# Performance work log

Measured on AMD Instinct MI355X. Metric: run time of the kernel, lower is better.

Reference implementation:

```python
import jax, jax.numpy as jnp
import numpy as np

B, P, M, N, H, K, EH = 16, 50, 512, 1024, 64, 20, 200


def setup_inputs() -> dict:
    key = jax.random.key(0)
    ks = jax.random.split(key, 16)
    b = jax.random.normal(ks[0], (B, P, M, 1), jnp.float32)
    A = jax.random.normal(ks[1], (1, P, M, N), jnp.float32) / np.float32(np.sqrt(M))
    # random undirected multigraph on P nodes, stored with both directions
    s = jax.random.randint(ks[2], (B, EH), 0, P)
    off = jax.random.randint(ks[3], (B, EH), 1, P)
    d = (s + off) % P
    edge_index = jnp.stack([jnp.concatenate([s, d], 1), jnp.concatenate([d, s], 1)], 1).astype(jnp.int32)  # [B,2,2*EH]

    def lin(k, fi, fo, scale=None):
        scale = np.float32(1.0 / np.sqrt(fi)) if scale is None else np.float32(scale)
        return jax.random.normal(k, (fi, fo), jnp.float32) * scale, jnp.zeros((fo,), jnp.float32)

    W_e1, b_e1 = lin(ks[4], P * M, P * H)
    W_e2, b_e2 = lin(ks[5], P * H, 2 * P * H)
    W_e3, b_e3 = lin(ks[6], 2 * P * H, 4 * P * H)
    W_c1, b_c1 = lin(ks[7], 4 * H, 2 * H)
    W_c2, b_c2 = lin(ks[8], 2 * H, 2 * H)
    W_f1, b_f1 = lin(ks[9], 2 * H, H)
    W_f2, _ = lin(ks[10], H, K * 4, scale=1e-3)
    b_f2 = jnp.full((K * 4,), -2.0, jnp.float32)  # mimics fc2 init (tiny weights, negative bias)
    max_param = jnp.array([0.01, 0.1, 0.1, 0.1], jnp.float32).reshape(1, 1, 1, 4)  # [alpha,tau,rho,eta]_max
    y0 = jax.random.normal(ks[11], (B, P, N, 1), jnp.float32) * 0.01
    u0 = jax.random.normal(ks[12], (B, P, N, 1), jnp.float32) * 0.01
    d0 = jax.random.normal(ks[13], (B, P, N, 1), jnp.float32) * 0.01
    return dict(b=b, A=A, edge_index=edge_index, max_param=max_param,
                W_e1=W_e1, b_e1=b_e1, W_e2=W_e2, b_e2=b_e2, W_e3=W_e3, b_e3=b_e3,
                W_c1=W_c1, b_c1=b_c1, W_c2=W_c2, b_c2=b_c2,
                W_f1=W_f1, b_f1=b_f1, W_f2=W_f2, b_f2=b_f2,
                y0=y0, u0=u0, d0=d0)


def _lrelu(x):
    return jax.nn.leaky_relu(x, 0.01)


def _gcn(x, s, d, W, bias):
    # GCNConv: sym-normalized propagation with self loops. x: [P,F]
    h = x @ W
    deg = jnp.zeros((x.shape[0],), x.dtype).at[d].add(1.0) + 1.0  # +1 self loop
    dinv = jax.lax.rsqrt(deg)
    agg = jnp.zeros_like(h).at[d].add(h[s] * (dinv[s] * dinv[d])[:, None])
    agg = agg + h * (dinv * dinv)[:, None]  # self-loop term
    return agg + bias


def _delta(y, s, d):
    # nested neighbor loop: for each directed edge (s,d): delta[s]+=y[s]-y[d]; delta[d]-=same
    diff = y[s] - y[d]  # [E,N,1]
    return jnp.zeros_like(y).at[s].add(diff).at[d].add(-diff)


def reference(b, A, edge_index, max_param,
              W_e1, b_e1, W_e2, b_e2, W_e3, b_e3,
              W_c1, b_c1, W_c2, b_c2, W_f1, b_f1, W_f2, b_f2,
              y0, u0, d0):
    Bb = b.shape[0]
    n = A.shape[3]
    k_steps = W_f2.shape[1] // 4
    src, dst = edge_index[:, 0], edge_index[:, 1]

    # ---- GNN hypernetwork ----
    x = b.reshape(Bb, -1)
    x = _lrelu(x @ W_e1 + b_e1)
    x = _lrelu(x @ W_e2 + b_e2)
    x = (x @ W_e3 + b_e3).reshape(Bb, P, -1)  # [B,P,4H]
    x = _lrelu(jax.vmap(lambda xf, s, d: _gcn(xf, s, d, W_c1, b_c1))(x, src, dst))
    x = _lrelu(jax.vmap(lambda xf, s, d: _gcn(xf, s, d, W_c2, b_c2))(x, src, dst))
    x = x.mean(axis=1)  # global_mean_pool over nodes
    x = _lrelu(x @ W_f1 + b_f1)
    hyp = (x @ W_f2 + b_f2).reshape(Bb, k_steps, 1, 4)
    hyp = jax.nn.sigmoid(jnp.cumsum(hyp, axis=1)) * max_param  # [B,K,1,4]
    hyp_scan = jnp.transpose(hyp, (1, 3, 0, 2))[..., None, None]  # [K,4,B,1,1,1]

    # ---- precompute ----
    A0 = A[0]  # [P,M,N]
    AtA = jnp.einsum('pmn,pmk->pnk', A0, A0)  # [P,N,N]
    Atb = jnp.einsum('pmn,bpmo->bpno', A0, b)  # [B,P,N,1]
    sum_nb = jax.vmap(lambda s: jnp.zeros((P,), b.dtype).at[s].add(1.0))(src)[:, :, None, None]  # [B,P,1,1]

    # ---- unrolled D-ADMM / DLASSO ----
    def step(carry, hk):
        y_k, U_k, dlt = carry
        alpha, tau, rho, eta = hk[0], hk[1], hk[2], hk[3]
        AtAy = jnp.einsum('pnk,bpko->bpno', AtA, y_k)
        g = AtAy - Atb + jnp.sign(y_k) * tau + U_k * sum_nb + dlt * rho
        y_n = y_k - alpha * g
        dlt_n = jax.vmap(_delta)(y_n, src, dst)
        U_n = U_k + dlt_n * eta
        return (y_n, U_n, dlt_n), y_n

    _, Y = jax.lax.scan(step, (y0, u0, d0), hyp_scan)
    return Y  # [K,B,P,N,1]
```

## Files before the change

### kernel.cpp

```cpp
#include <hip/hip_runtime.h>

namespace {
constexpr int NB = 16;
constexpr int NP = 50;
constexpr int NM = 512;
constexpr int NN = 1024;
constexpr int NK = 20;
constexpr long ASZ = (long)NP * NM * NN;
constexpr long YSZ = (long)NB * NP * NN;
}

typedef __attribute__((ext_vector_type(8))) short bf16x8;
typedef __attribute__((ext_vector_type(4))) float f32x4;

__device__ __forceinline__ float lrelu(float x){ return x > 0.f ? x : 0.01f*x; }
__device__ __forceinline__ float bfu(unsigned short x){
  unsigned v = ((unsigned)x) << 16;
  return __builtin_bit_cast(float, v);
}
__device__ __forceinline__ unsigned short f2bf(float f){
  unsigned u = __builtin_bit_cast(unsigned, f);
  u += 0x7fffu + ((u >> 16) & 1u);
  return (unsigned short)(u >> 16);
}
__device__ __forceinline__ long toff(int n, int kk){
  return (long)(n>>4)*16384 + (long)(kk>>5)*512 + (long)((n&15)*32 + ((kk>>3)&3)*8 + (kk&7));
}

__global__ __launch_bounds__(256) void k_prep(const float* __restrict__ A,
                      unsigned short* __restrict__ abfT){
  const int p = blockIdx.x, mt = blockIdx.y, nt = blockIdx.z;
  const int tid = threadIdx.x;
  __shared__ unsigned short tile[64][72];
  const int m0 = mt*64, n0 = nt*64;
  {
    int r = tid>>2, cs = (tid&3)*16;
    const float* src = A + ((long)p*NM + m0 + r)*NN + n0 + cs;
    unsigned short tmp[16];
    #pragma unroll
    for (int q=0;q<16;q+=4){
      float4 v = *(const float4*)(src+q);
      tmp[q+0]=f2bf(v.x); tmp[q+1]=f2bf(v.y); tmp[q+2]=f2bf(v.z); tmp[q+3]=f2bf(v.w);
    }
    #pragma unroll
    for (int q=0;q<16;q++) tile[r][cs+q] = tmp[q];
  }
  __syncthreads();
  {
    int r = tid>>2, cs = (tid&3)*16;
    unsigned short* dst = abfT + ((long)p*NN + n0 + r)*NM + m0 + cs;
    unsigned short tmp[16];
    #pragma unroll
    for (int q=0;q<16;q++) tmp[q] = tile[cs+q][r];
    #pragma unroll
    for (int q=0;q<16;q+=8) *(uint4*)(dst+q) = *(const uint4*)&tmp[q];
  }
}

__global__ void k_init(const float* __restrict__ y0, float* __restrict__ y,
                       unsigned short* __restrict__ ybf, int n){
  int e = (blockIdx.x*blockDim.x + threadIdx.x)*4;
  if (e >= n) return;
  float4 a = *(const float4*)(y0+e);
  *(float4*)(y+e) = a;
  ushort4 o; o.x=f2bf(a.x); o.y=f2bf(a.y); o.z=f2bf(a.z); o.w=f2bf(a.w);
  *(ushort4*)(ybf+e) = o;
}

__global__ __launch_bounds__(256) void k_e0(const float* __restrict__ u0,
      const float* __restrict__ d0, const float* __restrict__ atb,
      const float* __restrict__ snbg, const float* __restrict__ hypg,
      float* __restrict__ w, float* __restrict__ e){
  long i = ((long)blockIdx.x*256 + threadIdx.x)*4;
  if (i >= YSZ) return;
  long bp = i >> 10;
  int b = (int)(bp/NP), p = (int)(bp%NP);
  float sp = snbg[b*NP+p], rho = hypg[b*80 + 2];
  float4 uv = *(const float4*)(u0+i);
  float4 dv = *(const float4*)(d0+i);
  float4 av = *(const float4*)(atb+i);
  float4 wv, ev;
  wv.x = uv.x*sp - av.x; wv.y = uv.y*sp - av.y;
  wv.z = uv.z*sp - av.z; wv.w = uv.w*sp - av.w;
  ev.x = wv.x + dv.x*rho; ev.y = wv.y + dv.y*rho;
  ev.z = wv.z + dv.z*rho; ev.w = wv.w + dv.w*rho;
  *(float4*)(w+i) = wv;
  *(float4*)(e+i) = ev;
}

__global__ __launch_bounds__(256) void k_atb(const unsigned short* __restrict__ abfT,
                      const float* __restrict__ src, float* __restrict__ z){
  const int p = blockIdx.x;
  const int tid = threadIdx.x, wave = tid>>6, lane = tid&63;
  __shared__ unsigned short tlds[16][520];
  {
    int b = tid>>4, c0 = (tid&15)*8;
    const float* tr = src + ((long)b*NP + p)*NM;
    #pragma unroll
    for (int it=0; it<4; it++){
      float4 lo = *(const float4*)(tr + it*128 + c0);
      float4 hi = *(const float4*)(tr + it*128 + c0 + 4);
      unsigned short w[8];
      w[0]=f2bf(lo.x); w[1]=f2bf(lo.y); w[2]=f2bf(lo.z); w[3]=f2bf(lo.w);
      w[4]=f2bf(hi.x); w[5]=f2bf(hi.y); w[6]=f2bf(hi.z); w[7]=f2bf(hi.w);
      *(uint4*)&tlds[b][it*128 + c0] = *(const uint4*)w;
    }
  }
  __syncthreads();
  const int lr = lane&15, kg = lane>>4;
  const int nt0 = blockIdx.y*4 + wave;
  const int n0 = nt0*16, n1 = (nt0+32)*16;
  const unsigned short* b0 = abfT + ((long)p*NN + n0 + lr)*NM + kg*8;
  const unsigned short* b1 = abfT + ((long)p*NN + n1 + lr)*NM + kg*8;
  const unsigned short* tp = &tlds[lr][kg*8];
  f32x4 acc0a={0.f,0.f,0.f,0.f}, acc0b={0.f,0.f,0.f,0.f};
  f32x4 acc1a={0.f,0.f,0.f,0.f}, acc1b={0.f,0.f,0.f,0.f};
  #pragma unroll 4
  for (int ks=0; ks<16; ks+=2){
    bf16x8 t0 = *(const bf16x8*)(tp + ks*32);
    bf16x8 t1 = *(const bf16x8*)(tp + ks*32 + 32);
    bf16x8 b00 = *(const bf16x8*)(b0 + (long)ks*32);
    bf16x8 b01 = *(const bf16x8*)(b0 + (long)ks*32 + 32);
    bf16x8 b10 = *(const bf16x8*)(b1 + (long)ks*32);
    bf16x8 b11 = *(const bf16x8*)(b1 + (long)ks*32 + 32);
    acc0a = __builtin_amdgcn_mfma_f32_16x16x32_bf16(t0, b00, acc0a, 0, 0, 0);
    acc1a = __builtin_amdgcn_mfma_f32_16x16x32_bf16(t0, b10, acc1a, 0, 0, 0);
    acc0b = __builtin_amdgcn_mfma_f32_16x16x32_bf16(t1, b01, acc0b, 0, 0, 0);
    acc1b = __builtin_amdgcn_mfma_f32_16x16x32_bf16(t1, b11, acc1b, 0, 0, 0);
  }
  f32x4 acc0 = acc0a + acc0b;
  f32x4 acc1 = acc1a + acc1b;
  #pragma unroll
  for (int r=0;r<4;r++){
    int bb = kg*4 + r;
    z[((long)bb*NP + p)*NN + n0 + lr] = acc0[r];
    z[((long)bb*NP + p)*NN + n1 + lr] = acc1[r];
  }
}

__global__ __launch_bounds__(256) void k_ata(const unsigned short* __restrict__ abfT,
                      unsigned short* __restrict__ ata){
  const int p = blockIdx.y;
  int yy = blockIdx.x, bi = 0;
  while (yy >= 8 - bi){ yy -= 8 - bi; bi++; }
  const int bj = bi + yy;
  const int i0 = bi*128, j0 = bj*128;
  const int tid = threadIdx.x, wave = tid>>6, lane = tid&63;
  const int lr = lane&15, kg = lane>>4;
  __shared__ unsigned short pa[128][72];
  __shared__ unsigned short pb[128][72];
  f32x4 acc[2][8];
  #pragma unroll
  for (int ti=0;ti<2;ti++)
    #pragma unroll
    for (int tj=0;tj<8;tj++) acc[ti][tj] = (f32x4){0.f,0.f,0.f,0.f};
  const unsigned short* Abase = abfT + (long)p*NN*NM;
  for (int mc=0; mc<NM; mc+=64){
    __syncthreads();
    {
      int r = tid>>1, c0 = (tid&1)*32;
      const unsigned short* sa = Abase + (long)(i0 + r)*NM + mc + c0;
      const unsigned short* sb = Abase + (long)(j0 + r)*NM + mc + c0;
      #pragma unroll
      for (int q=0;q<32;q+=8){
        *(uint4*)&pa[r][c0+q] = *(const uint4*)(sa+q);
        *(uint4*)&pb[r][c0+q] = *(const uint4*)(sb+q);
      }
    }
    __syncthreads();
    #pragma unroll
    for (int ks=0; ks<2; ks++){
      bf16x8 av0 = *(const bf16x8*)&pa[wave*32      + lr][ks*32 + kg*8];
      bf16x8 av1 = *(const bf16x8*)&pa[wave*32 + 16 + lr][ks*32 + kg*8];
      #pragma unroll
      for (int tj=0;tj<8;tj++){
        bf16x8 bv = *(const bf16x8*)&pb[tj*16 + lr][ks*32 + kg*8];
        acc[0][tj] = __builtin_amdgcn_mfma_f32_16x16x32_bf16(av0, bv, acc[0][tj], 0,0,0);
        acc[1][tj] = __builtin_amdgcn_mfma_f32_16x16x32_bf16(av1, bv, acc[1][tj], 0,0,0);
      }
    }
  }
  const long pbase = (long)p << 20;
  #pragma unroll
  for (int ti=0; ti<2; ti++){
    const int ib = i0 + wave*32 + ti*16;
    #pragma unroll
    for (int tj=0; tj<8; tj++){
      const int jb = j0 + tj*16;
      unsigned short w[4];
      #pragma unroll
      for (int r=0;r<4;r++) w[r] = f2bf(acc[ti][tj][r]);
      #pragma unroll
      for (int r=0;r<4;r++)
        ata[pbase + toff(ib + kg*4 + r, jb + lr)] = w[r];
      if (bi != bj){
        #pragma unroll
        for (int r=0;r<4;r++)
          ata[pbase + toff(jb + lr, ib + kg*4 + r)] = w[r];
      }
    }
  }
}

__global__ __launch_bounds__(256) void k_enc2(const float* __restrict__ X, const float* __restrict__ W,
                           float* __restrict__ part, int fi, int fo, int ichunk, int actin){
  const int tid = threadIdx.x;
  const int o0 = (blockIdx.x*256 + tid)*4;
  const int c  = blockIdx.y;
  const bool ok = o0 < fo;
  __shared__ float xs[64][16];
  float4 acc[16];
  #pragma unroll
  for (int b=0;b<16;b++){ acc[b].x=0.f; acc[b].y=0.f; acc[b].z=0.f; acc[b].w=0.f; }
  const long ibase = (long)c*ichunk;
  const int xb = tid&15, xio = (tid>>4)*4;
  for (int s=0; s<ichunk; s+=64){
    float4 v = *(const float4*)(X + (long)xb*fi + ibase + s + xio);
    if (actin){ v.x=lrelu(v.x); v.y=lrelu(v.y); v.z=lrelu(v.z); v.w=lrelu(v.w); }
    __syncthreads();
    xs[xio+0][xb]=v.x; xs[xio+1][xb]=v.y; xs[xio+2][xb]=v.z; xs[xio+3][xb]=v.w;
    __syncthreads();
    const float* wp = W + (ibase+s)*fo + o0;
    #pragma unroll 4
    for (int i=0;i<64;i++){
      float4 w;
      if (ok) w = *(const float4*)(wp + (long)i*fo);
      else { w.x=0.f; w.y=0.f; w.z=0.f; w.w=0.f; }
      #pragma unroll
      for (int b2=0;b2<16;b2+=4){
        float4 x4 = *(const float4*)&xs[i][b2];
        acc[b2+0].x += w.x*x4.x; acc[b2+0].y += w.y*x4.x; acc[b2+0].z += w.z*x4.x; acc[b2+0].w += w.w*x4.x;
        acc[b2+1].x += w.x*x4.y; acc[b2+1].y += w.y*x4.y; acc[b2+1].z += w.z*x4.y; acc[b2+1].w += w.w*x4.y;
        acc[b2+2].x += w.x*x4.z; acc[b2+2].y += w.y*x4.z; acc[b2+2].z += w.z*x4.z; acc[b2+2].w += w.w*x4.z;
        acc[b2+3].x += w.x*x4.w; acc[b2+3].y += w.y*x4.w; acc[b2+3].z += w.z*x4.w; acc[b2+3].w += w.w*x4.w;
      }
    }
  }
  if (ok){
    float* pp = part + ((long)c*16)*fo + o0;
    #pragma unroll
    for (int b=0;b<16;b++) *(float4*)(pp + (long)b*fo) = acc[b];
  }
}

__global__ void k_enc_reduce(const float* __restrict__ part, const float* __restrict__ bias,
                             float* __restrict__ out, int fo, int nchunk){
  int i = blockIdx.x*256 + threadIdx.x;
  if (i >= 16*fo) return;
  int o = i % fo;
  float s = bias[o];
  for (int c=0;c<nchunk;c++) s += part[(long)c*16*fo + i];
  out[i] = s;
}

__global__ __launch_bounds__(64) void k_graph(const int* __restrict__ ei, float* __restrict__ adjg,
                        float* __restrict__ dmg, float* __restrict__ snbg){
  const int b = blockIdx.x, tid = threadIdx.x;
  __shared__ float adj[2500], dm[2500], deg[50], dinv[50], snb[50];
  for (int i=tid;i<2500;i+=64){ adj[i]=0.f; dm[i]=0.f; }
  if (tid<50){ deg[tid]=0.f; snb[tid]=0.f; }
  __syncthreads();
  const int* e = ei + b*800;
  for (int k=tid;k<400;k+=64){
    atomicAdd(&deg[e[400+k]], 1.f);
    atomicAdd(&snb[e[k]], 1.f);
  }
  __syncthreads();
  if (tid<50) dinv[tid] = 1.f / sqrtf(deg[tid] + 1.f);
  __syncthreads();
  for (int k=tid;k<400;k+=64){
    int s = e[k], d = e[400+k];
    atomicAdd(&adj[d*50+s], dinv[s]*dinv[d]);
    atomicAdd(&dm[s*50+s],  1.f); atomicAdd(&dm[s*50+d], -1.f);
    atomicAdd(&dm[d*50+d],  1.f); atomicAdd(&dm[d*50+s], -1.f);
  }
  __syncthreads();
  if (tid<50) adj[tid*50+tid] += dinv[tid]*dinv[tid];
  __syncthreads();
  for (int i=tid;i<2500;i+=64){ adjg[b*2500+i]=adj[i]; dmg[b*2500+i]=dm[i]; }
  if (tid<50) snbg[b*50+tid]=snb[tid];
}

__global__ __launch_bounds__(256) void k_gnn(const float* __restrict__ h3,
     const float* __restrict__ Wc1, const float* __restrict__ bc1,
     const float* __restrict__ Wc2, const float* __restrict__ bc2,
     const float* __restrict__ Wf1, const float* __restrict__ bf1,
     const float* __restrict__ Wf2, const float* __restrict__ bf2,
     const float* __restrict__ maxp, const float* __restrict__ adjg,
     float* __restrict__ hypg){
  const int b = blockIdx.x, tid = threadIdx.x;
  __shared__ float adj[2500];
  __shared__ float bufA[6400];
  __shared__ float bufB[6400];
  __shared__ float xm[128], hv1[64], raw[80];
  for (int i=tid;i<2500;i+=256) adj[i] = adjg[b*2500+i];

  const int j = tid & 127, nh = tid >> 7;
  float acc[25];
  #pragma unroll
  for (int q=0;q<25;q++) acc[q]=0.f;
  for (int ic=0; ic<4; ic++){
    __syncthreads();
    for (int e=tid; e<800; e+=256){
      int n = e>>4, seg = (e&15)*4;
      *(float4*)&bufB[n*64+seg] = *(const float4*)(h3 + (long)b*12800 + n*256 + ic*64 + seg);
    }
    __syncthreads();
    for (int i=0;i<64;i+=4){
      float w0 = Wc1[(long)(ic*64+i+0)*128 + j];
      float w1 = Wc1[(long)(ic*64+i+1)*128 + j];
      float w2 = Wc1[(long)(ic*64+i+2)*128 + j];
      float w3 = Wc1[(long)(ic*64+i+3)*128 + j];
      #pragma unroll
      for (int q=0;q<25;q++){
        float4 xv = *(const float4*)&bufB[(nh*25+q)*64 + i];
        acc[q] += xv.x*w0 + xv.y*w1 + xv.z*w2 + xv.w*w3;
      }
    }
  }
  __syncthreads();
  #pragma unroll
  for (int q=0;q<25;q++) bufA[(nh*25+q)*128 + j] = acc[q];
  __syncthreads();
  {
    float a2[25];
    float bv = bc1[j];
    #pragma unroll
    for (int q=0;q<25;q++) a2[q]=bv;
    for (int qq=0; qq<50; qq++){
      float hvv = bufA[qq*128 + j];
      #pragma unroll
      for (int q=0;q<25;q++) a2[q] += adj[(nh*25+q)*50 + qq]*hvv;
    }
    __syncthreads();
    #pragma unroll
    for (int q=0;q<25;q++) bufB[(nh*25+q)*128 + j] = lrelu(a2[q]);
  }
  __syncthreads();
  {
    float a2[25];
    #pragma unroll
    for (int q=0;q<25;q++) a2[q]=0.f;
    for (int i=0;i<128;i+=4){
      float w0 = Wc2[(long)(i+0)*128 + j];
      float w1 = Wc2[(long)(i+1)*128 + j];
      float w2 = Wc2[(long)(i+2)*128 + j];
      float w3 = Wc2[(long)(i+3)*128 + j];
      #pragma unroll
      for (int q=0;q<25;q++){
        float4 xv = *(const float4*)&bufB[(nh*25+q)*128 + i];
        a2[q] += xv.x*w0 + xv.y*w1 + xv.z*w2 + xv.w*w3;
      }
    }
    __syncthreads();
    #pragma unroll
    for (int q=0;q<25;q++) bufA[(nh*25+q)*128 + j] = a2[q];
  }
  __syncthreads();
  {
    float a2[25];
    float bv = bc2[j];
    #pragma unroll
    for (int q=0;q<25;q++) a2[q]=bv;
    for (int qq=0; qq<50; qq++){
      float hvv = bufA[qq*128 + j];
      #pragma unroll
      for (int q=0;q<25;q++) a2[q] += adj[(nh*25+q)*50 + qq]*hvv;
    }
    __syncthreads();
    #pragma unroll
    for (int q=0;q<25;q++) bufB[(nh*25+q)*128 + j] = lrelu(a2[q]);
  }
  __syncthreads();
  if (tid < 128){
    float s = 0.f;
    for (int n=0;n<50;n++) s += bufB[n*128 + tid];
    xm[tid] = s * (1.f/50.f);
  }
  __syncthreads();
  if (tid < 64){
    float s = bf1[tid];
    for (int i=0;i<128;i++) s += xm[i]*Wf1[i*64 + tid];
    hv1[tid] = lrelu(s);
  }
  __syncthreads();
  if (tid < 80){
    float s = bf2[tid];
    for (int i=0;i<64;i++) s += hv1[i]*Wf2[i*80 + tid];
    raw[tid] = s;
  }
  __syncthreads();
  if (tid < 4){
    float c = 0.f;
    for (int k=0;k<20;k++){
      c += raw[k*4 + tid];
      hypg[b*80 + k*4 + tid] = maxp[tid] / (1.f + expf(-c));
    }
  }
}

__global__ __launch_bounds__(256, 4) void k_z(const unsigned short* __restrict__ ata,
      const unsigned short* __restrict__ ybin, const float* __restrict__ ebuf,
      const float* __restrict__ hypg, int k,
      float* __restrict__ y, unsigned short* __restrict__ ybout,
      float* __restrict__ yout){
  const int p = blockIdx.x;
  const int tid = threadIdx.x, wave = tid>>6, lane = tid&63;
  __shared__ unsigned short ylds[16][1032];
  {
    int b = tid>>4, c0 = (tid&15)*8;
    const unsigned short* yr = ybin + ((long)b*NP + p)*NN;
    #pragma unroll
    for (int it=0; it<8; it++)
      *(uint4*)&ylds[b][it*128 + c0] = *(const uint4*)(yr + it*128 + c0);
  }
  const int lr = lane&15, kg = lane>>4;
  const int t  = blockIdx.y*4 + wave;
  const int n0 = t*16;
  const unsigned short* bp = ata + ((long)p<<20) + (long)t*16384 + lr*32 + kg*8;
  const unsigned short* yp = &ylds[lr][kg*8];

  bf16x8 B[3][4];
  #pragma unroll
  for (int j=0;j<4;j++) B[0][j] = *(const bf16x8*)(bp + (0*4+j)*512);
  #pragma unroll
  for (int j=0;j<4;j++) B[1][j] = *(const bf16x8*)(bp + (1*4+j)*512);

  float yv4[4], e4[4];
  float4 hp4[4];
  #pragma unroll
  for (int r=0;r<4;r++){
    const int b = kg*4 + r;
    const long idx = ((long)b*NP + p)*NN + n0 + lr;
    yv4[r] = y[idx]; e4[r] = ebuf[idx];
    hp4[r] = *(const float4*)(hypg + b*80 + k*4);
  }
  __syncthreads();

  f32x4 a0={0.f,0.f,0.f,0.f}, a1={0.f,0.f,0.f,0.f}, a2={0.f,0.f,0.f,0.f}, a3={0.f,0.f,0.f,0.f};
  #pragma unroll
  for (int i=0;i<8;i++){
    const int cur = i % 3;
    const int nxt = (i+2) % 3;
    if (i < 6){
      #pragma unroll
      for (int j=0;j<4;j++) B[nxt][j] = *(const bf16x8*)(bp + ((i+2)*4+j)*512);
    }
    bf16x8 q0 = *(const bf16x8*)(yp + (i*4+0)*32);
    bf16x8 q1 = *(const bf16x8*)(yp + (i*4+1)*32);
    bf16x8 q2 = *(const bf16x8*)(yp + (i*4+2)*32);
    bf16x8 q3 = *(const bf16x8*)(yp + (i*4+3)*32);
    a0 = __builtin_amdgcn_mfma_f32_16x16x32_bf16(q0, B[cur][0], a0, 0,0,0);
    a1 = __builtin_amdgcn_mfma_f32_16x16x32_bf16(q1, B[cur][1], a1, 0,0,0);
    a2 = __builtin_amdgcn_mfma_f32_16x16x32_bf16(q2, B[cur][2], a2, 0,0,0);
    a3 = __builtin_amdgcn_mfma_f32_16x16x32_bf16(q3, B[cur][3], a3, 0,0,0);
  }
  f32x4 z = (a0 + a1) + (a2 + a3);
  #pragma unroll
  for (int r=0;r<4;r++){
    const int b = kg*4 + r;
    const long idx = ((long)b*NP + p)*NN + n0 + lr;
    float yv = yv4[r];
    float g = z[r] + ((yv>0.f)?1.f:((yv<0.f)?-1.f:0.f))*hp4[r].y + e4[r];
    float ynv = yv - hp4[r].x*g;
    y[idx] = ynv; ybout[idx] = f2bf(ynv); yout[(long)k*YSZ + idx] = ynv;
  }
}

__global__ __launch_bounds__(256) void k_dm(const float* __restrict__ dmg,
      const float* __restrict__ snbg, const float* __restrict__ hypg, int k,
      const unsigned short* __restrict__ ybf, float* __restrict__ w, float* __restrict__ e){
  const int b = blockIdx.x, n0 = blockIdx.y*128, tid = threadIdx.x;
  __shared__ float ys[50][128];
  __shared__ float dms[2500];
  for (int i=tid;i<2500;i+=256) dms[i] = dmg[b*2500+i];
  for (int i=tid; i<6400; i+=256){
    int p=i>>7, nn=i&127;
    ys[p][nn] = bfu(ybf[((long)b*NP+p)*NN + n0 + nn]);
  }
  __syncthreads();
  const float eta = hypg[b*80 + k*4 + 3];
  const float rhon = hypg[b*80 + (k+1)*4 + 2];
  for (int i=tid; i<6400; i+=256){
    int p=i>>7, nn=i&127;
    float s=0.f;
    #pragma unroll 10
    for (int q=0;q<NP;q++) s += dms[p*50+q]*ys[q][nn];
    long idx = ((long)b*NP+p)*NN + n0 + nn;
    float wn = w[idx] + s*eta*snbg[b*NP+p];
    w[idx] = wn;
    e[idx] = wn + s*rhon;
  }
}

extern "C" void kernel_launch(void* const* d_in, const int* in_sizes, int n_in,
                              void* d_out, int out_size, void* d_ws, size_t ws_size,
                              hipStream_t stream){
  (void)in_sizes; (void)n_in; (void)out_size; (void)ws_size;
  const float* bin = (const float*)d_in[0];
  const float* A   = (const float*)d_in[1];
  const int*   ei  = (const int*)d_in[2];
  const float* mxp = (const float*)d_in[3];
  const float* We1 = (const float*)d_in[4];  const float* be1 = (const float*)d_in[5];
  const float* We2 = (const float*)d_in[6];  const float* be2 = (const float*)d_in[7];
  const float* We3 = (const float*)d_in[8];  const float* be3 = (const float*)d_in[9];
  const float* Wc1 = (const float*)d_in[10]; const float* bc1 = (const float*)d_in[11];
  const float* Wc2 = (const float*)d_in[12]; const float* bc2 = (const float*)d_in[13];
  const float* Wf1 = (const float*)d_in[14]; const float* bf1 = (const float*)d_in[15];
  const float* Wf2 = (const float*)d_in[16]; const float* bf2 = (const float*)d_in[17];
  const float* y0  = (const float*)d_in[18];
  const float* u0  = (const float*)d_in[19];
  const float* dd0 = (const float*)d_in[20];
  float* out = (float*)d_out;

  char* cur = (char*)d_ws;
  auto alloc = [&](size_t bytes)->void*{
    void* pp = (void*)cur; cur += (bytes + 255) & ~(size_t)255; return pp;
  };
  unsigned short* abfT = (unsigned short*)alloc(ASZ*2);
  unsigned short* ata  = (unsigned short*)alloc((size_t)NP*1024*1024*2);
  float* atb = (float*)alloc(YSZ*4);
  float* y   = (float*)alloc(YSZ*4);
  unsigned short* ybf0 = (unsigned short*)alloc(YSZ*2);
  unsigned short* ybf1 = (unsigned short*)alloc(YSZ*2);
  float* w   = (float*)alloc(YSZ*4);
  float* eb  = (float*)alloc(YSZ*4);
  float* h1  = (float*)alloc((size_t)16*3200*4);
  float* h2  = (float*)alloc((size_t)16*6400*4);
  float* h3  = (float*)alloc((size_t)16*12800*4);
  float* adj = (float*)alloc((size_t)16*2500*4);
  float* dm  = (float*)alloc((size_t)16*2500*4);
  float* snb = (float*)alloc((size_t)16*50*4);
  float* hyp = (float*)alloc((size_t)16*80*4);
  float* part= (float*)alloc((size_t)84000000);

  k_prep<<<dim3(50,8,16), dim3(256), 0, stream>>>(A, abfT);
  k_init<<<dim3(800), dim3(256), 0, stream>>>(y0, y, ybf0, (int)YSZ);
  k_atb<<<dim3(50,8), dim3(256), 0, stream>>>(abfT, bin, atb);
  k_ata<<<dim3(36,50), dim3(256), 0, stream>>>(abfT, ata);

  k_enc2<<<dim3(4,200),  dim3(256), 0, stream>>>(bin, We1, part, 25600, 3200, 128, 0);
  k_enc_reduce<<<dim3(200), dim3(256), 0, stream>>>(part, be1, h1, 3200, 200);
  k_enc2<<<dim3(7,50),  dim3(256), 0, stream>>>(h1, We2, part, 3200, 6400, 64, 1);
  k_enc_reduce<<<dim3(400), dim3(256), 0, stream>>>(part, be2, h2, 6400, 50);
  k_enc2<<<dim3(13,100), dim3(256), 0, stream>>>(h2, We3, part, 6400, 12800, 64, 1);
  k_enc_reduce<<<dim3(800), dim3(256), 0, stream>>>(part, be3, h3, 12800, 100);

  k_graph<<<dim3(16), dim3(64), 0, stream>>>(ei, adj, dm, snb);
  k_gnn<<<dim3(16), dim3(256), 0, stream>>>(h3, Wc1, bc1, Wc2, bc2, Wf1, bf1, Wf2, bf2, mxp, adj, hyp);
  k_e0<<<dim3(800), dim3(256), 0, stream>>>(u0, dd0, atb, snb, hyp, w, eb);

  for (int k=0;k<NK;k++){
    const unsigned short* ybin = (k & 1) ? ybf1 : ybf0;
    unsigned short* ybout      = (k & 1) ? ybf0 : ybf1;
    k_z<<<dim3(50,16), dim3(256), 0, stream>>>(ata, ybin, eb, hyp, k, y, ybout, out);
    if (k < NK-1){
      const unsigned short* ybnew = (k & 1) ? ybf0 : ybf1;
      k_dm<<<dim3(16,8), dim3(256), 0, stream>>>(dm, snb, hyp, k, ybnew, w, eb);
    }
  }
}
```

Baseline: 1.485 ms.

## Fuse graph-difference update into the per-step AtA GEMV kernel

Removes the separate k_dm launch per unrolled step. The graph-Laplacian product over neighbours (dm times y) is now computed inside the AtA step kernel from the previous bf16 iterate, and the dual w update is folded in as well, so the e buffer and its global round-trip go away. Each block redundantly reloads a 50-node slice of y for its 64 columns. Launch bounds drop to 2 blocks per CU because of the larger LDS footprint. This halves the launches per step and cuts global traffic, but adds redundant neighbour loads and extra syncs inside the GEMV kernel.

After: 2.675 ms. 1.8x slower.

```diff
diff --git a/kernel.cpp b/kernel.cpp
--- a/kernel.cpp
+++ b/kernel.cpp
@@ -67,25 +67,20 @@
   *(ushort4*)(ybf+e) = o;
 }
 
-__global__ __launch_bounds__(256) void k_e0(const float* __restrict__ u0,
-      const float* __restrict__ d0, const float* __restrict__ atb,
-      const float* __restrict__ snbg, const float* __restrict__ hypg,
-      float* __restrict__ w, float* __restrict__ e){
+__global__ __launch_bounds__(256) void k_w0(const float* __restrict__ u0,
+      const float* __restrict__ atb, const float* __restrict__ snbg,
+      float* __restrict__ w){
   long i = ((long)blockIdx.x*256 + threadIdx.x)*4;
   if (i >= YSZ) return;
   long bp = i >> 10;
   int b = (int)(bp/NP), p = (int)(bp%NP);
-  float sp = snbg[b*NP+p], rho = hypg[b*80 + 2];
+  float sp = snbg[b*NP+p];
   float4 uv = *(const float4*)(u0+i);
-  float4 dv = *(const float4*)(d0+i);
   float4 av = *(const float4*)(atb+i);
-  float4 wv, ev;
+  float4 wv;
   wv.x = uv.x*sp - av.x; wv.y = uv.y*sp - av.y;
   wv.z = uv.z*sp - av.z; wv.w = uv.w*sp - av.w;
-  ev.x = wv.x + dv.x*rho; ev.y = wv.y + dv.y*rho;
-  ev.z = wv.z + dv.z*rho; ev.w = wv.w + dv.w*rho;
   *(float4*)(w+i) = wv;
-  *(float4*)(e+i) = ev;
 }
 
 __global__ __launch_bounds__(256) void k_atb(const unsigned short* __restrict__ abfT,
@@ -399,14 +394,26 @@
   }
 }
 
-__global__ __launch_bounds__(256, 4) void k_z(const unsigned short* __restrict__ ata,
-      const unsigned short* __restrict__ ybin, const float* __restrict__ ebuf,
+__global__ __launch_bounds__(256, 2) void k_z2(const unsigned short* __restrict__ ata,
+      const unsigned short* __restrict__ ybin, const float* __restrict__ d0,
+      const float* __restrict__ dmg, const float* __restrict__ snbg,
       const float* __restrict__ hypg, int k,
-      float* __restrict__ y, unsigned short* __restrict__ ybout,
-      float* __restrict__ yout){
+      float* __restrict__ y, float* __restrict__ w,
+      unsigned short* __restrict__ ybout, float* __restrict__ yout){
   const int p = blockIdx.x;
+  const int ng = blockIdx.y;
   const int tid = threadIdx.x, wave = tid>>6, lane = tid&63;
+  const int lr = lane&15, kg = lane>>4;
   __shared__ unsigned short ylds[16][1032];
+  __shared__ unsigned short ybq[16][16][66];
+  __shared__ float dmp[16][52];
+  __shared__ float snp[16];
+
+  for (int e2=tid; e2<800; e2+=256){
+    int b=e2/50, q=e2%50;
+    dmp[b][q] = dmg[b*2500 + p*50 + q];
+  }
+  if (tid<16) snp[tid] = snbg[tid*NP + p];
   {
     int b = tid>>4, c0 = (tid&15)*8;
     const unsigned short* yr = ybin + ((long)b*NP + p)*NN;
@@ -414,8 +421,36 @@
     for (int it=0; it<8; it++)
       *(uint4*)&ylds[b][it*128 + c0] = *(const uint4*)(yr + it*128 + c0);
   }
-  const int lr = lane&15, kg = lane>>4;
-  const int t  = blockIdx.y*4 + wave;
+
+  const int nl = wave*16 + lr;
+  float dlt[4] = {0.f,0.f,0.f,0.f};
+  if (k == 0){
+    #pragma unroll
+    for (int r=0;r<4;r++)
+      dlt[r] = d0[((long)(kg*4+r)*NP + p)*NN + ng*64 + nl];
+  } else {
+    for (int qc=0; qc<50; qc+=16){
+      const int qn = (50-qc < 16) ? (50-qc) : 16;
+      __syncthreads();
+      for (int rr = tid>>3; rr < qn*16; rr += 32){
+        int q = rr >> 4, b = rr & 15;
+        int c8 = (tid&7)*8;
+        const unsigned short* src = ybin + ((long)b*NP + (qc+q))*NN + ng*64 + c8;
+        *(uint4*)&ybq[q][b][c8] = *(const uint4*)src;
+      }
+      __syncthreads();
+      #pragma unroll
+      for (int r=0;r<4;r++){
+        int b = kg*4+r;
+        float s = 0.f;
+        for (int q=0;q<qn;q++)
+          s += dmp[b][qc+q] * bfu(ybq[q][b][nl]);
+        dlt[r] += s;
+      }
+    }
+  }
+
+  const int t  = ng*4 + wave;
   const int n0 = t*16;
   const unsigned short* bp = ata + ((long)p<<20) + (long)t*16384 + lr*32 + kg*8;
   const unsigned short* yp = &ylds[lr][kg*8];
@@ -426,14 +461,16 @@
   #pragma unroll
   for (int j=0;j<4;j++) B[1][j] = *(const bf16x8*)(bp + (1*4+j)*512);
 
-  float yv4[4], e4[4];
+  float yv4[4], wv4[4];
   float4 hp4[4];
+  float etap[4];
   #pragma unroll
   for (int r=0;r<4;r++){
     const int b = kg*4 + r;
     const long idx = ((long)b*NP + p)*NN + n0 + lr;
-    yv4[r] = y[idx]; e4[r] = ebuf[idx];
+    yv4[r] = y[idx]; wv4[r] = w[idx];
     hp4[r] = *(const float4*)(hypg + b*80 + k*4);
+    etap[r] = (k > 0) ? hypg[b*80 + (k-1)*4 + 3] : 0.f;
   }
   __syncthreads();
 
@@ -460,36 +497,13 @@
   for (int r=0;r<4;r++){
     const int b = kg*4 + r;
     const long idx = ((long)b*NP + p)*NN + n0 + lr;
+    float wn = wv4[r] + dlt[r]*etap[r]*snp[b];
+    if (k > 0) w[idx] = wn;
+    float e = wn + dlt[r]*hp4[r].z;
     float yv = yv4[r];
-    float g = z[r] + ((yv>0.f)?1.f:((yv<0.f)?-1.f:0.f))*hp4[r].y + e4[r];
+    float g = z[r] + ((yv>0.f)?1.f:((yv<0.f)?-1.f:0.f))*hp4[r].y + e;
     float ynv = yv - hp4[r].x*g;
     y[idx] = ynv; ybout[idx] = f2bf(ynv); yout[(long)k*YSZ + idx] = ynv;
-  }
-}
-
-__global__ __launch_bounds__(256) void k_dm(const float* __restrict__ dmg,
-      const float* __restrict__ snbg, const float* __restrict__ hypg, int k,
-      const unsigned short* __restrict__ ybf, float* __restrict__ w, float* __restrict__ e){
-  const int b = blockIdx.x, n0 = blockIdx.y*128, tid = threadIdx.x;
-  __shared__ float ys[50][128];
-  __shared__ float dms[2500];
-  for (int i=tid;i<2500;i+=256) dms[i] = dmg[b*2500+i];
-  for (int i=tid; i<6400; i+=256){
-    int p=i>>7, nn=i&127;
-    ys[p][nn] = bfu(ybf[((long)b*NP+p)*NN + n0 + nn]);
-  }
-  __syncthreads();
-  const float eta = hypg[b*80 + k*4 + 3];
-  const float rhon = hypg[b*80 + (k+1)*4 + 2];
-  for (int i=tid; i<6400; i+=256){
-    int p=i>>7, nn=i&127;
-    float s=0.f;
-    #pragma unroll 10
-    for (int q=0;q<NP;q++) s += dms[p*50+q]*ys[q][nn];
-    long idx = ((long)b*NP+p)*NN + n0 + nn;
-    float wn = w[idx] + s*eta*snbg[b*NP+p];
-    w[idx] = wn;
-    e[idx] = wn + s*rhon;
   }
 }
 
@@ -524,7 +538,6 @@
   unsigned short* ybf0 = (unsigned short*)alloc(YSZ*2);
   unsigned short* ybf1 = (unsigned short*)alloc(YSZ*2);
   float* w   = (float*)alloc(YSZ*4);
-  float* eb  = (float*)alloc(YSZ*4);
   float* h1  = (float*)alloc((size_t)16*3200*4);
   float* h2  = (float*)alloc((size_t)16*6400*4);
   float* h3  = (float*)alloc((size_t)16*12800*4);
@@ -548,15 +561,12 @@
 
   k_graph<<<dim3(16), dim3(64), 0, stream>>>(ei, adj, dm, snb);
   k_gnn<<<dim3(16), dim3(256), 0, stream>>>(h3, Wc1, bc1, Wc2, bc2, Wf1, bf1, Wf2, bf2, mxp, adj, hyp);
-  k_e0<<<dim3(800), dim3(256), 0, stream>>>(u0, dd0, atb, snb, hyp, w, eb);
+  k_w0<<<dim3(800), dim3(256), 0, stream>>>(u0, atb, snb, w);
 
   for (int k=0;k<NK;k++){
     const unsigned short* ybin = (k & 1) ? ybf1 : ybf0;
     unsigned short* ybout      = (k & 1) ? ybf0 : ybf1;
-    k_z<<<dim3(50,16), dim3(256), 0, stream>>>(ata, ybin, eb, hyp, k, y, ybout, out);
-    if (k < NK-1){
-      const unsigned short* ybnew = (k & 1) ? ybf0 : ybf1;
-      k_dm<<<dim3(16,8), dim3(256), 0, stream>>>(dm, snb, hyp, k, ybnew, w, eb);
-    }
-  }
-}
+    k_z2<<<dim3(50,16), dim3(256), 0, stream>>>(ata, ybin, dd0, dm, snb, hyp, k,
+                                                y, w, ybout, out);
+  }
+}
```
